# Optimization experiments

Hardware: AMD Instinct MI355X
Metric: run time of the kernel (lower is better)

Reference implementation:

```python
import jax, jax.numpy as jnp
import numpy as np

B, S, D, H = 2, 2048, 1024, 16
DK = D // H

def setup_inputs() -> dict:
    key = jax.random.key(0)
    ks = jax.random.split(key, 8)
    return {
        "query": jax.random.normal(ks[0], (B, S, D), dtype=jnp.float32),
        "key": jax.random.normal(ks[1], (B, S, D), dtype=jnp.float32),
        "value": jax.random.normal(ks[2], (B, S, D), dtype=jnp.float32),
        "mask": jax.random.randint(ks[3], (B, S, S), 0, 2, dtype=jnp.int32),
        "w_q": jax.random.normal(ks[4], (D, D), dtype=jnp.float32) * (D ** -0.5),
        "w_k": jax.random.normal(ks[5], (D, D), dtype=jnp.float32) * (D ** -0.5),
        "w_v": jax.random.normal(ks[6], (D, D), dtype=jnp.float32) * (D ** -0.5),
        "w_o": jax.random.normal(ks[7], (D, D), dtype=jnp.float32) * (D ** -0.5),
    }

def reference(query, key, value, mask, w_q, w_k, w_v, w_o):
    b, s, d = query.shape
    # Linear projections (torch nn.Linear: x @ W.T); here w_* are [out, in]
    Q = jnp.einsum('bsd,ed->bse', query, w_q).reshape(b, s, H, DK).transpose(0, 2, 1, 3)
    K = jnp.einsum('bsd,ed->bse', key, w_k).reshape(b, s, H, DK).transpose(0, 2, 1, 3)
    V = jnp.einsum('bsd,ed->bse', value, w_v).reshape(b, s, H, DK).transpose(0, 2, 1, 3)
    scale = jnp.float32(DK ** 0.5)
    scores = jnp.einsum('bhqd,bhkd->bhqk', Q, K) / scale  # [B,H,S,S]
    scores = jnp.where(mask[:, None, :, :] == 0, jnp.float32(-1e9), scores)
    attn = jax.nn.softmax(scores, axis=-1)  # dropout p=0 -> identity
    out = jnp.einsum('bhqk,bhkd->bhqd', attn, V)  # [B,H,S,DK]
    out = out.transpose(0, 2, 1, 3).reshape(b, s, d)
    return jnp.einsum('bsd,ed->bse', out, w_o)
```

## Files before the change

### kernel.cpp

```cpp
#include <hip/hip_runtime.h>
#include <stdint.h>

#define B_ 2
#define S_ 2048
#define D_ 1024
#define H_ 16
#define DK_ 64

typedef __attribute__((ext_vector_type(8))) short short8;
typedef __attribute__((ext_vector_type(4))) float f32x4;

__device__ __forceinline__ short f2bf(float f) {
    uint32_t u = __float_as_uint(f);
    return (short)((u + 0x7FFFu + ((u >> 16) & 1u)) >> 16);
}

__device__ __forceinline__ float fexp2(float x) {
    float r;
    asm("v_exp_f32 %0, %1" : "=v"(r) : "v"(x));
    return r;
}

__device__ __forceinline__ uint32_t cvt_pk_bf16(float lo, float hi) {
    uint32_t r;
    asm("v_cvt_pk_bf16_f32 %0, %1, %2" : "=v"(r) : "v"(lo), "v"(hi));
    return r;
}

#define GLOAD16(gptr, lptr)                                                      \
    __builtin_amdgcn_global_load_lds(                                            \
        (const __attribute__((address_space(1))) void*)(gptr),                   \
        (__attribute__((address_space(3))) void*)(lptr), 16, 0, 0)

__global__ __launch_bounds__(256) void cast_qkv(const float* __restrict__ a,
                                                const float* __restrict__ b,
                                                const float* __restrict__ c,
                                                short* __restrict__ oa,
                                                short* __restrict__ ob,
                                                short* __restrict__ oc) {
    int bid = blockIdx.x;
    int sel = bid >> 11;
    int i = (bid & 2047) * 256 + threadIdx.x;
    const float* in = (sel == 0) ? a : (sel == 1) ? b : c;
    short* out = (sel == 0) ? oa : (sel == 1) ? ob : oc;
    const float4* p = ((const float4*)in) + (size_t)i * 2;
    float4 x = p[0], y = p[1];
    short8 o;
    o[0] = f2bf(x.x); o[1] = f2bf(x.y); o[2] = f2bf(x.z); o[3] = f2bf(x.w);
    o[4] = f2bf(y.x); o[5] = f2bf(y.y); o[6] = f2bf(y.z); o[7] = f2bf(y.w);
    *(((short8*)out) + i) = o;
}

__global__ __launch_bounds__(256) void cast_w4(const float* __restrict__ a,
                                               const float* __restrict__ b,
                                               const float* __restrict__ c,
                                               const float* __restrict__ d,
                                               short* __restrict__ oa,
                                               short* __restrict__ ob,
                                               short* __restrict__ oc,
                                               short* __restrict__ od) {
    int bid = blockIdx.x;
    int sel = bid >> 9;
    int i = (bid & 511) * 256 + threadIdx.x;
    const float* in = (sel == 0) ? a : (sel == 1) ? b : (sel == 2) ? c : d;
    short* out = (sel == 0) ? oa : (sel == 1) ? ob : (sel == 2) ? oc : od;
    const float4* p = ((const float4*)in) + (size_t)i * 2;
    float4 x = p[0], y = p[1];
    short8 o;
    o[0] = f2bf(x.x); o[1] = f2bf(x.y); o[2] = f2bf(x.z); o[3] = f2bf(x.w);
    o[4] = f2bf(y.x); o[5] = f2bf(y.y); o[6] = f2bf(y.z); o[7] = f2bf(y.w);
    *(((short8*)out) + i) = o;
}

__global__ __launch_bounds__(256) void pack_mask(const int* __restrict__ mask,
                                                 uint32_t* __restrict__ packed,
                                                 float* __restrict__ lut) {
    if (blockIdx.x == 0 && threadIdx.x < 64) {
        int e = threadIdx.x >> 2, r = threadIdx.x & 3;
        lut[threadIdx.x] = __int_as_float(((e >> r) & 1) ? 0x7F800000u : 0xFF800000u);
    }
    size_t t = (size_t)blockIdx.x * 256 + threadIdx.x;
    int4 m = ((const int4*)mask)[t];
    uint32_t nib = (m.x != 0 ? 1u : 0u) | (m.y != 0 ? 2u : 0u) |
                   (m.z != 0 ? 4u : 0u) | (m.w != 0 ? 8u : 0u);
    int lane = threadIdx.x & 63;
    uint32_t v = nib << ((lane & 7) * 4);
    v |= __shfl_xor(v, 1);
    v |= __shfl_xor(v, 2);
    v |= __shfl_xor(v, 4);
    if ((lane & 7) == 0) packed[t >> 3] = v;
}

#define GEMM_BODY(A, W, C, F32OUT, Mv, Nv, Kv)                                              \
    __shared__ short As[128 * 32];                                                          \
    __shared__ short Bs[128 * 32];                                                          \
    const int tid = threadIdx.x;                                                            \
    const int lane = tid & 63;                                                              \
    const int w = tid >> 6;                                                                 \
    const int wm = w >> 1, wn = w & 1;                                                      \
    const int l_ = blockIdx.x + (blockIdx.y << 3);                                          \
    const int xcd_ = l_ & 7, ii_ = l_ >> 3;                                                 \
    const int mBase = ((xcd_ << 2) + (ii_ >> 3)) * 128;                                     \
    const int nBase = (ii_ & 7) * 128;                                                      \
    f32x4 acc[4][4];                                                                        \
    _Pragma("unroll") for (int i = 0; i < 4; i++)                                           \
        _Pragma("unroll") for (int j = 0; j < 4; j++) acc[i][j] = (f32x4)0.f;               \
    const int srow = lane >> 2;                                                             \
    const int sslot = lane & 3;                                                             \
    for (int k0 = 0; k0 < Kv; k0 += 32) {                                                   \
        _Pragma("unroll") for (int i = 0; i < 2; ++i) {                                     \
            int seg = w * 2 + i;                                                            \
            int row = seg * 16 + srow;                                                      \
            const short* ga = A + (size_t)(mBase + row) * Kv + k0 + sslot * 8;              \
            GLOAD16(ga, (char*)As + seg * 1024);                                            \
            const short* gb = W + (size_t)(nBase + row) * Kv + k0 + sslot * 8;              \
            GLOAD16(gb, (char*)Bs + seg * 1024);                                            \
        }                                                                                   \
        asm volatile("s_waitcnt vmcnt(0)" ::: "memory");                                    \
        __syncthreads();                                                                    \
        short8 af[4], bfv[4];                                                               \
        _Pragma("unroll") for (int mi = 0; mi < 4; mi++)                                    \
            af[mi] = *(const short8*)&As[(wm * 64 + mi * 16 + (lane & 15)) * 32 + (lane >> 4) * 8]; \
        _Pragma("unroll") for (int ni = 0; ni < 4; ni++)                                    \
            bfv[ni] = *(const short8*)&Bs[(wn * 64 + ni * 16 + (lane & 15)) * 32 + (lane >> 4) * 8]; \
        _Pragma("unroll") for (int mi = 0; mi < 4; mi++)                                    \
            _Pragma("unroll") for (int ni = 0; ni < 4; ni++)                                \
                acc[mi][ni] = __builtin_amdgcn_mfma_f32_16x16x32_bf16(af[mi], bfv[ni], acc[mi][ni], 0, 0, 0); \
        __syncthreads();                                                                    \
    }                                                                                       \
    _Pragma("unroll") for (int mi = 0; mi < 4; mi++)                                        \
        _Pragma("unroll") for (int ni = 0; ni < 4; ni++)                                    \
            _Pragma("unroll") for (int r = 0; r < 4; r++) {                                 \
                int row = mBase + wm * 64 + mi * 16 + (lane >> 4) * 4 + r;                  \
                int col = nBase + wn * 64 + ni * 16 + (lane & 15);                          \
                float v = acc[mi][ni][r];                                                   \
                if (F32OUT) ((float*)C)[(size_t)row * Nv + col] = v;                        \
                else        ((short*)C)[(size_t)row * Nv + col] = f2bf(v);                  \
            }

__global__ __launch_bounds__(256) void gemm3_nt(const short* __restrict__ A0, const short* __restrict__ W0, short* __restrict__ C0,
                                                const short* __restrict__ A1, const short* __restrict__ W1, short* __restrict__ C1,
                                                const short* __restrict__ A2, const short* __restrict__ W2, short* __restrict__ C2) {
    const int z = blockIdx.z;
    const short* A = (z == 0) ? A0 : (z == 1) ? A1 : A2;
    const short* W = (z == 0) ? W0 : (z == 1) ? W1 : W2;
    short* C = (z == 0) ? C0 : (z == 1) ? C1 : C2;
    GEMM_BODY(A, W, C, 0, (B_ * S_), D_, D_)
}

__global__ __launch_bounds__(256) void gemm_out(const short* __restrict__ A,
                                                const short* __restrict__ W,
                                                float* __restrict__ C) {
    GEMM_BODY(A, W, C, 1, (B_ * S_), D_, D_)
}

__global__ __launch_bounds__(256) void transpose_v(const short* __restrict__ Vp,
                                                   short* __restrict__ Vt) {
    __shared__ short t[64 * 72];
    int bid = blockIdx.x;
    int bh = bid >> 5;
    int st = bid & 31;
    int b = bh >> 4, h = bh & 15;
    int sBase = st * 64;
    int tid = threadIdx.x;
#pragma unroll
    for (int i = 0; i < 2; i++) {
        int ci = i * 256 + tid;
        int sr = ci >> 3, sl = ci & 7;
        short8 v = *(const short8*)&Vp[(size_t)(b * S_ + sBase + sr) * D_ + h * 64 + sl * 8];
#pragma unroll
        for (int j = 0; j < 8; j++) t[(sl * 8 + j) * 72 + sr] = v[j];
    }
    __syncthreads();
#pragma unroll
    for (int i = 0; i < 2; i++) {
        int ci = i * 256 + tid;
        int dk = ci >> 3, sl = ci & 7;
        short8 o = *(const short8*)&t[dk * 72 + sl * 8];
        *(short8*)&Vt[(size_t)((b * H_ + h) * 64 + dk) * S_ + sBase + sl * 8] = o;
    }
}

__global__ __launch_bounds__(256) void attn_kernel(const short* __restrict__ Qp,
                                                   const short* __restrict__ Kp,
                                                   const short* __restrict__ Vt,
                                                   const uint32_t* __restrict__ mp,
                                                   const float* __restrict__ lutg,
                                                   short* __restrict__ Op) {
    __shared__ short Ks[2][64 * 64];
    __shared__ short Vs[2][64 * 64];
    const int l_ = blockIdx.x + (blockIdx.y << 5);
    const int bh = ((l_ & 7) << 2) + (l_ >> 8);
    const int qt = (l_ >> 3) & 31;
    const int b = bh >> 4, h = bh & 15;
    const int qBase = qt * 64;
    const int tid = threadIdx.x, lane = tid & 63, w = tid >> 6;
    const int lg = lane >> 4;
    const int li = lane & 15;
    const float c1 = 0.18033688011112042f;

    const int q = qBase + w * 16 + li;

    short8 qf[2];
#pragma unroll
    for (int ks = 0; ks < 2; ks++)
        qf[ks] = *(const short8*)&Qp[(size_t)(b * S_ + q) * D_ + h * 64 + lg * 8 + ks * 32];

    const int r0 = tid >> 3, sl = tid & 7;
    const int gs = sl ^ (r0 & 7);
    const short* kg0 = Kp + ((size_t)(b * S_) + r0) * D_ + h * 64 + gs * 8;
    const short* kg1 = kg0 + (size_t)32 * D_;
    const short* vg0 = Vt + ((size_t)bh * 64 + r0) * S_ + gs * 8;
    const short* vg1 = vg0 + (size_t)32 * S_;
    const uint32_t* mrow = mp + ((size_t)(b * S_) + q) * 64;
    char* ldsK = (char*)&Ks[0][0];
    char* ldsV = (char*)&Vs[0][0];
    const int woff = w * 1024;

    GLOAD16(kg0, ldsK + woff);
    GLOAD16(kg1, ldsK + 4096 + woff);
    GLOAD16(vg0, ldsV + woff);
    GLOAD16(vg1, ldsV + 4096 + woff);
    uint2 mw = *(const uint2*)mrow;
    asm volatile("s_waitcnt vmcnt(0)" ::: "memory");
    __syncthreads();

    float m_r = -1e30f, l_r = 0.f;
    f32x4 acc[4];
#pragma unroll
    for (int g = 0; g < 4; g++) acc[g] = (f32x4)0.f;

    int cur = 0;

    for (int kt = 0; kt < S_ / 64; ++kt) {
        f32x4 msk[4];
#pragma unroll
        for (int nt = 0; nt < 4; nt++) {
            uint32_t wd = (nt < 2) ? mw.x : mw.y;
            uint32_t nib = (wd >> (((nt & 1) << 4) + (lg << 2))) & 0xFu;
            msk[nt] = *(const f32x4*)&lutg[nib * 4];
        }

        uint2 mwn;
        if (kt < S_ / 64 - 1) {
            const size_t ko = (size_t)((kt + 1) * 64) * D_;
            const int vo = (kt + 1) * 64;
            const int boff = (cur ^ 1) * 8192 + woff;
            GLOAD16(kg0 + ko, ldsK + boff);
            GLOAD16(kg1 + ko, ldsK + boff + 4096);
            GLOAD16(vg0 + vo, ldsV + boff);
            GLOAD16(vg1 + vo, ldsV + boff + 4096);
            mwn = *(const uint2*)&mrow[(kt + 1) * 2];
        }

        f32x4 sc[4];
        __builtin_amdgcn_s_setprio(1);
#pragma unroll
        for (int nt = 0; nt < 4; nt++) {
            f32x4 c = (f32x4)0.f;
#pragma unroll
            for (int ks = 0; ks < 2; ks++) {
                short8 kf = *(const short8*)&Ks[cur][(nt * 16 + li) * 64 + (((lg + ks * 4) ^ (li & 7)) << 3)];
                c = __builtin_amdgcn_mfma_f32_16x16x32_bf16(kf, qf[ks], c, 0, 0, 0);
            }
            sc[nt] = c;
        }
        __builtin_amdgcn_s_setprio(0);

        float tm = fmaxf(fmaxf(fmaxf(sc[0][0], sc[0][1]), fmaxf(sc[0][2], sc[0][3])),
                         fmaxf(fmaxf(sc[1][0], sc[1][1]), fmaxf(sc[1][2], sc[1][3])));
        tm = fmaxf(tm, fmaxf(fmaxf(fmaxf(sc[2][0], sc[2][1]), fmaxf(sc[2][2], sc[2][3])),
                             fmaxf(fmaxf(sc[3][0], sc[3][1]), fmaxf(sc[3][2], sc[3][3]))));
        tm = fmaxf(tm, __shfl_xor(tm, 16));
        tm = fmaxf(tm, __shfl_xor(tm, 32));

        if (__any((tm - m_r) * c1 > 10.0f)) {
            float mn = fmaxf(m_r, tm);
            float alpha = fexp2((m_r - mn) * c1);
            m_r = mn;
            l_r *= alpha;
#pragma unroll
            for (int g = 0; g < 4; g++) acc[g] *= alpha;
        }
        float mc = m_r * c1;

        uint32_t u[4][2];
        float ls = 0.f;
#pragma unroll
        for (int nt = 0; nt < 4; nt++) {
            float e0 = fexp2(fminf(__builtin_fmaf(sc[nt][0], c1, -mc), msk[nt][0]));
            float e1 = fexp2(fminf(__builtin_fmaf(sc[nt][1], c1, -mc), msk[nt][1]));
            float e2 = fexp2(fminf(__builtin_fmaf(sc[nt][2], c1, -mc), msk[nt][2]));
            float e3 = fexp2(fminf(__builtin_fmaf(sc[nt][3], c1, -mc), msk[nt][3]));
            ls += (e0 + e1) + (e2 + e3);
            u[nt][0] = cvt_pk_bf16(e0, e1);
            u[nt][1] = cvt_pk_bf16(e2, e3);
        }
        ls += __shfl_xor(ls, 16);
        ls += __shfl_xor(ls, 32);
        l_r += ls;

        __builtin_amdgcn_s_setprio(1);
#pragma unroll
        for (int ks = 0; ks < 2; ks++) {
            const uint32_t s00 = u[2 * ks][0], s01 = u[2 * ks][1];
            const uint32_t s10 = u[2 * ks + 1][0], s11 = u[2 * ks + 1][1];
            uint32_t e0 = (lg & 1) ? s00 : s10;
            uint32_t e1 = (lg & 1) ? s01 : s11;
            uint32_t x0 = (uint32_t)__shfl_xor((int)e0, 16);
            uint32_t x1 = (uint32_t)__shfl_xor((int)e1, 16);
            union { uint32_t w4[4]; short8 s8; } pu;
            pu.w4[0] = (lg & 1) ? x0 : s00;
            pu.w4[1] = (lg & 1) ? x1 : s01;
            pu.w4[2] = (lg & 1) ? s10 : x0;
            pu.w4[3] = (lg & 1) ? s11 : x1;
            const int f = ks * 4 + ((lg & 1) << 1) + (lg >> 1);
#pragma unroll
            for (int g = 0; g < 4; g++) {
                short8 vf = *(const short8*)&Vs[cur][(g * 16 + li) * 64 + ((f ^ (li & 7)) << 3)];
                acc[g] = __builtin_amdgcn_mfma_f32_16x16x32_bf16(vf, pu.s8, acc[g], 0, 0, 0);
            }
        }
        __builtin_amdgcn_s_setprio(0);

        asm volatile("s_waitcnt vmcnt(0)" ::: "memory");
        __syncthreads();
        cur ^= 1;
        if (kt < S_ / 64 - 1) mw = mwn;
    }

    float inv = 1.f / l_r;
    short* orow = &Op[(size_t)(b * S_ + q) * D_ + h * 64];
#pragma unroll
    for (int g = 0; g < 4; g++) {
        uint2 o;
        o.x = cvt_pk_bf16(acc[g][0] * inv, acc[g][1] * inv);
        o.y = cvt_pk_bf16(acc[g][2] * inv, acc[g][3] * inv);
        *(uint2*)&orow[g * 16 + lg * 4] = o;
    }
}

extern "C" void kernel_launch(void* const* d_in, const int* in_sizes, int n_in,
                              void* d_out, int out_size, void* d_ws, size_t ws_size,
                              hipStream_t stream) {
    const float* q  = (const float*)d_in[0];
    const float* k  = (const float*)d_in[1];
    const float* v  = (const float*)d_in[2];
    const int*   mk = (const int*)d_in[3];
    const float* wq = (const float*)d_in[4];
    const float* wk = (const float*)d_in[5];
    const float* wv = (const float*)d_in[6];
    const float* wo = (const float*)d_in[7];

    const size_t SZ = (size_t)B_ * S_ * D_;
    const size_t DD = (size_t)D_ * D_;
    const size_t NEED = (6 * SZ + 4 * DD) * 2 + (size_t)B_ * S_ * 64 * 4 + 256;
    if (ws_size < NEED) return;

    short* ws  = (short*)d_ws;
    short* qb  = ws;
    short* kb  = qb + SZ;
    short* vb  = kb + SZ;
    short* wqb = vb + SZ;
    short* wkb = wqb + DD;
    short* wvb = wkb + DD;
    short* wob = wvb + DD;
    short* Qp  = wob + DD;
    short* Kp  = Qp + SZ;
    short* Vp  = Kp + SZ;
    uint32_t* mp = (uint32_t*)(Vp + SZ);
    float* lutg = (float*)(mp + (size_t)B_ * S_ * 64);
    short* Vtr = qb;
    short* Opx = kb;

    dim3 blk(256);
    cast_qkv<<<dim3(3 * 2048), blk, 0, stream>>>(q, k, v, qb, kb, vb);
    cast_w4<<<dim3(4 * 512), blk, 0, stream>>>(wq, wk, wv, wo, wqb, wkb, wvb, wob);
    pack_mask<<<dim3((unsigned)((size_t)B_ * S_ * S_ / 4 / 256)), blk, 0, stream>>>(mk, mp, lutg);

    gemm3_nt<<<dim3(D_ / 128, B_ * S_ / 128, 3), blk, 0, stream>>>(
        qb, wqb, Qp, kb, wkb, Kp, vb, wvb, Vp);

    transpose_v<<<dim3(B_ * H_ * (S_ / 64)), blk, 0, stream>>>(Vp, Vtr);

    attn_kernel<<<dim3(32, 32), blk, 0, stream>>>(Qp, Kp, Vtr, mp, lutg, Opx);

    gemm_out<<<dim3(D_ / 128, B_ * S_ / 128), blk, 0, stream>>>(Opx, wob, (float*)d_out);
}
```

Measured before the change: 171.7 us.

## Fuse prep kernels, widen attention K/V tile to 128, fold mask into MFMA accumulator

Merges the three cast and mask-packing kernels into one prep launch, cutting launch overhead. The attention loop now processes 128 keys per iteration: two 64-row K/V sub-tiles per stage, double-buffered. The mask is applied as an additive bias (0 or -8e9) used as the MFMA initial accumulator, which removes the per-element fminf. This doubles LDS use per block and raises register pressure, which may reduce occupancy. Fully masked rows may also behave slightly differently from the -1e9 reference semantics.

Result: no change. 169.0 us (-1.5%).

```diff
diff --git a/kernel.cpp b/kernel.cpp
--- a/kernel.cpp
+++ b/kernel.cpp
@@ -32,63 +32,60 @@
         (const __attribute__((address_space(1))) void*)(gptr),                   \
         (__attribute__((address_space(3))) void*)(lptr), 16, 0, 0)
 
-__global__ __launch_bounds__(256) void cast_qkv(const float* __restrict__ a,
-                                                const float* __restrict__ b,
-                                                const float* __restrict__ c,
-                                                short* __restrict__ oa,
-                                                short* __restrict__ ob,
-                                                short* __restrict__ oc) {
+__global__ __launch_bounds__(256) void prep(const float* __restrict__ q,
+                                            const float* __restrict__ k,
+                                            const float* __restrict__ v,
+                                            const float* __restrict__ wq,
+                                            const float* __restrict__ wk,
+                                            const float* __restrict__ wv,
+                                            const float* __restrict__ wo,
+                                            const int* __restrict__ mask,
+                                            short* __restrict__ qb, short* __restrict__ kb,
+                                            short* __restrict__ vb,
+                                            short* __restrict__ wqb, short* __restrict__ wkb,
+                                            short* __restrict__ wvb, short* __restrict__ wob,
+                                            uint32_t* __restrict__ packed,
+                                            float* __restrict__ lut) {
     int bid = blockIdx.x;
-    int sel = bid >> 11;
-    int i = (bid & 2047) * 256 + threadIdx.x;
-    const float* in = (sel == 0) ? a : (sel == 1) ? b : c;
-    short* out = (sel == 0) ? oa : (sel == 1) ? ob : oc;
-    const float4* p = ((const float4*)in) + (size_t)i * 2;
-    float4 x = p[0], y = p[1];
-    short8 o;
-    o[0] = f2bf(x.x); o[1] = f2bf(x.y); o[2] = f2bf(x.z); o[3] = f2bf(x.w);
-    o[4] = f2bf(y.x); o[5] = f2bf(y.y); o[6] = f2bf(y.z); o[7] = f2bf(y.w);
-    *(((short8*)out) + i) = o;
-}
-
-__global__ __launch_bounds__(256) void cast_w4(const float* __restrict__ a,
-                                               const float* __restrict__ b,
-                                               const float* __restrict__ c,
-                                               const float* __restrict__ d,
-                                               short* __restrict__ oa,
-                                               short* __restrict__ ob,
-                                               short* __restrict__ oc,
-                                               short* __restrict__ od) {
-    int bid = blockIdx.x;
-    int sel = bid >> 9;
-    int i = (bid & 511) * 256 + threadIdx.x;
-    const float* in = (sel == 0) ? a : (sel == 1) ? b : (sel == 2) ? c : d;
-    short* out = (sel == 0) ? oa : (sel == 1) ? ob : (sel == 2) ? oc : od;
-    const float4* p = ((const float4*)in) + (size_t)i * 2;
-    float4 x = p[0], y = p[1];
-    short8 o;
-    o[0] = f2bf(x.x); o[1] = f2bf(x.y); o[2] = f2bf(x.z); o[3] = f2bf(x.w);
-    o[4] = f2bf(y.x); o[5] = f2bf(y.y); o[6] = f2bf(y.z); o[7] = f2bf(y.w);
-    *(((short8*)out) + i) = o;
-}
-
-__global__ __launch_bounds__(256) void pack_mask(const int* __restrict__ mask,
-                                                 uint32_t* __restrict__ packed,
-                                                 float* __restrict__ lut) {
-    if (blockIdx.x == 0 && threadIdx.x < 64) {
-        int e = threadIdx.x >> 2, r = threadIdx.x & 3;
-        lut[threadIdx.x] = __int_as_float(((e >> r) & 1) ? 0x7F800000u : 0xFF800000u);
-    }
-    size_t t = (size_t)blockIdx.x * 256 + threadIdx.x;
-    int4 m = ((const int4*)mask)[t];
-    uint32_t nib = (m.x != 0 ? 1u : 0u) | (m.y != 0 ? 2u : 0u) |
-                   (m.z != 0 ? 4u : 0u) | (m.w != 0 ? 8u : 0u);
-    int lane = threadIdx.x & 63;
-    uint32_t v = nib << ((lane & 7) * 4);
-    v |= __shfl_xor(v, 1);
-    v |= __shfl_xor(v, 2);
-    v |= __shfl_xor(v, 4);
-    if ((lane & 7) == 0) packed[t >> 3] = v;
+    int tid = threadIdx.x;
+    if (bid < 8192) {
+        const float* in;
+        short* out;
+        int i;
+        if (bid < 6144) {
+            int sel = bid >> 11;
+            i = (bid & 2047) * 256 + tid;
+            in = (sel == 0) ? q : (sel == 1) ? k : v;
+            out = (sel == 0) ? qb : (sel == 1) ? kb : vb;
+        } else {
+            int idx = bid - 6144;
+            int sel = idx >> 9;
+            i = (idx & 511) * 256 + tid;
+            in = (sel == 0) ? wq : (sel == 1) ? wk : (sel == 2) ? wv : wo;
+            out = (sel == 0) ? wqb : (sel == 1) ? wkb : (sel == 2) ? wvb : wob;
+            if (idx == 0 && tid < 64) {
+                int e = tid >> 2, r = tid & 3;
+                lut[tid] = ((e >> r) & 1) ? 0.0f : -8.0e9f;
+            }
+        }
+        const float4* p = ((const float4*)in) + (size_t)i * 2;
+        float4 x = p[0], y = p[1];
+        short8 o;
+        o[0] = f2bf(x.x); o[1] = f2bf(x.y); o[2] = f2bf(x.z); o[3] = f2bf(x.w);
+        o[4] = f2bf(y.x); o[5] = f2bf(y.y); o[6] = f2bf(y.z); o[7] = f2bf(y.w);
+        *(((short8*)out) + i) = o;
+    } else {
+        size_t t = (size_t)(bid - 8192) * 256 + tid;
+        int4 m = ((const int4*)mask)[t];
+        uint32_t nib = (m.x != 0 ? 1u : 0u) | (m.y != 0 ? 2u : 0u) |
+                       (m.z != 0 ? 4u : 0u) | (m.w != 0 ? 8u : 0u);
+        int lane = tid & 63;
+        uint32_t vv = nib << ((lane & 7) * 4);
+        vv |= __shfl_xor(vv, 1);
+        vv |= __shfl_xor(vv, 2);
+        vv |= __shfl_xor(vv, 4);
+        if ((lane & 7) == 0) packed[t >> 3] = vv;
+    }
 }
 
 #define GEMM_BODY(A, W, C, F32OUT, Mv, Nv, Kv)                                              \
@@ -187,8 +184,8 @@
                                                    const uint32_t* __restrict__ mp,
                                                    const float* __restrict__ lutg,
                                                    short* __restrict__ Op) {
-    __shared__ short Ks[2][64 * 64];
-    __shared__ short Vs[2][64 * 64];
+    __shared__ short Ks[2][2][64 * 64];
+    __shared__ short Vs[2][2][64 * 64];
     const int l_ = blockIdx.x + (blockIdx.y << 5);
     const int bh = ((l_ & 7) << 2) + (l_ >> 8);
     const int qt = (l_ >> 3) & 31;
@@ -208,20 +205,21 @@
 
     const int r0 = tid >> 3, sl = tid & 7;
     const int gs = sl ^ (r0 & 7);
-    const short* kg0 = Kp + ((size_t)(b * S_) + r0) * D_ + h * 64 + gs * 8;
-    const short* kg1 = kg0 + (size_t)32 * D_;
-    const short* vg0 = Vt + ((size_t)bh * 64 + r0) * S_ + gs * 8;
-    const short* vg1 = vg0 + (size_t)32 * S_;
+    const short* kgb = Kp + ((size_t)(b * S_) + r0) * D_ + h * 64 + gs * 8;
+    const short* vgb = Vt + ((size_t)bh * 64 + r0) * S_ + gs * 8;
     const uint32_t* mrow = mp + ((size_t)(b * S_) + q) * 64;
-    char* ldsK = (char*)&Ks[0][0];
-    char* ldsV = (char*)&Vs[0][0];
+    char* ldsK = (char*)&Ks[0][0][0];
+    char* ldsV = (char*)&Vs[0][0][0];
     const int woff = w * 1024;
 
-    GLOAD16(kg0, ldsK + woff);
-    GLOAD16(kg1, ldsK + 4096 + woff);
-    GLOAD16(vg0, ldsV + woff);
-    GLOAD16(vg1, ldsV + 4096 + woff);
-    uint2 mw = *(const uint2*)mrow;
+#pragma unroll
+    for (int st = 0; st < 2; st++) {
+        GLOAD16(kgb + (size_t)(st * 64) * D_, ldsK + st * 8192 + woff);
+        GLOAD16(kgb + (size_t)(st * 64 + 32) * D_, ldsK + st * 8192 + 4096 + woff);
+        GLOAD16(vgb + st * 64, ldsV + st * 8192 + woff);
+        GLOAD16(vgb + st * 64 + (size_t)32 * S_, ldsV + st * 8192 + 4096 + woff);
+    }
+    uint4 mw4 = *(const uint4*)mrow;
     asm volatile("s_waitcnt vmcnt(0)" ::: "memory");
     __syncthreads();
 
@@ -232,45 +230,56 @@
 
     int cur = 0;
 
-    for (int kt = 0; kt < S_ / 64; ++kt) {
-        f32x4 msk[4];
-#pragma unroll
-        for (int nt = 0; nt < 4; nt++) {
-            uint32_t wd = (nt < 2) ? mw.x : mw.y;
+    for (int kt = 0; kt < S_ / 128; ++kt) {
+        uint32_t mwarr[4] = {mw4.x, mw4.y, mw4.z, mw4.w};
+        f32x4 msk[8];
+#pragma unroll
+        for (int nt = 0; nt < 8; nt++) {
+            uint32_t wd = mwarr[nt >> 1];
             uint32_t nib = (wd >> (((nt & 1) << 4) + (lg << 2))) & 0xFu;
             msk[nt] = *(const f32x4*)&lutg[nib * 4];
         }
 
-        uint2 mwn;
-        if (kt < S_ / 64 - 1) {
-            const size_t ko = (size_t)((kt + 1) * 64) * D_;
-            const int vo = (kt + 1) * 64;
-            const int boff = (cur ^ 1) * 8192 + woff;
-            GLOAD16(kg0 + ko, ldsK + boff);
-            GLOAD16(kg1 + ko, ldsK + boff + 4096);
-            GLOAD16(vg0 + vo, ldsV + boff);
-            GLOAD16(vg1 + vo, ldsV + boff + 4096);
-            mwn = *(const uint2*)&mrow[(kt + 1) * 2];
-        }
-
-        f32x4 sc[4];
+        uint4 mwn;
+        if (kt < S_ / 128 - 1) {
+            const int boff = (cur ^ 1) * 16384 + woff;
+#pragma unroll
+            for (int st = 0; st < 2; st++) {
+                const size_t kr = (size_t)((kt + 1) * 128 + st * 64);
+                GLOAD16(kgb + kr * D_, ldsK + boff + st * 8192);
+                GLOAD16(kgb + (kr + 32) * D_, ldsK + boff + st * 8192 + 4096);
+                GLOAD16(vgb + kr, ldsV + boff + st * 8192);
+                GLOAD16(vgb + kr + (size_t)32 * S_, ldsV + boff + st * 8192 + 4096);
+            }
+            mwn = *(const uint4*)&mrow[(kt + 1) * 4];
+        }
+
+        f32x4 sc[8];
         __builtin_amdgcn_s_setprio(1);
 #pragma unroll
-        for (int nt = 0; nt < 4; nt++) {
-            f32x4 c = (f32x4)0.f;
-#pragma unroll
-            for (int ks = 0; ks < 2; ks++) {
-                short8 kf = *(const short8*)&Ks[cur][(nt * 16 + li) * 64 + (((lg + ks * 4) ^ (li & 7)) << 3)];
-                c = __builtin_amdgcn_mfma_f32_16x16x32_bf16(kf, qf[ks], c, 0, 0, 0);
-            }
-            sc[nt] = c;
-        }
+        for (int st = 0; st < 2; st++)
+#pragma unroll
+            for (int ntl = 0; ntl < 4; ntl++) {
+                f32x4 c = msk[st * 4 + ntl];
+#pragma unroll
+                for (int ks = 0; ks < 2; ks++) {
+                    short8 kf = *(const short8*)&Ks[cur][st][(ntl * 16 + li) * 64 + (((lg + ks * 4) ^ (li & 7)) << 3)];
+                    c = __builtin_amdgcn_mfma_f32_16x16x32_bf16(kf, qf[ks], c, 0, 0, 0);
+                }
+                sc[st * 4 + ntl] = c;
+            }
         __builtin_amdgcn_s_setprio(0);
 
-        float tm = fmaxf(fmaxf(fmaxf(sc[0][0], sc[0][1]), fmaxf(sc[0][2], sc[0][3])),
-                         fmaxf(fmaxf(sc[1][0], sc[1][1]), fmaxf(sc[1][2], sc[1][3])));
-        tm = fmaxf(tm, fmaxf(fmaxf(fmaxf(sc[2][0], sc[2][1]), fmaxf(sc[2][2], sc[2][3])),
-                             fmaxf(fmaxf(sc[3][0], sc[3][1]), fmaxf(sc[3][2], sc[3][3]))));
+        float t0 = fmaxf(fmaxf(sc[0][0], sc[0][1]), fmaxf(sc[0][2], sc[0][3]));
+        float t1 = fmaxf(fmaxf(sc[1][0], sc[1][1]), fmaxf(sc[1][2], sc[1][3]));
+        float t2 = fmaxf(fmaxf(sc[2][0], sc[2][1]), fmaxf(sc[2][2], sc[2][3]));
+        float t3 = fmaxf(fmaxf(sc[3][0], sc[3][1]), fmaxf(sc[3][2], sc[3][3]));
+        float t4 = fmaxf(fmaxf(sc[4][0], sc[4][1]), fmaxf(sc[4][2], sc[4][3]));
+        float t5 = fmaxf(fmaxf(sc[5][0], sc[5][1]), fmaxf(sc[5][2], sc[5][3]));
+        float t6 = fmaxf(fmaxf(sc[6][0], sc[6][1]), fmaxf(sc[6][2], sc[6][3]));
+        float t7 = fmaxf(fmaxf(sc[7][0], sc[7][1]), fmaxf(sc[7][2], sc[7][3]));
+        float tm = fmaxf(fmaxf(fmaxf(t0, t1), fmaxf(t2, t3)),
+                         fmaxf(fmaxf(t4, t5), fmaxf(t6, t7)));
         tm = fmaxf(tm, __shfl_xor(tm, 16));
         tm = fmaxf(tm, __shfl_xor(tm, 32));
 
@@ -284,14 +293,14 @@
         }
         float mc = m_r * c1;
 
-        uint32_t u[4][2];
+        uint32_t u[8][2];
         float ls = 0.f;
 #pragma unroll
-        for (int nt = 0; nt < 4; nt++) {
-            float e0 = fexp2(fminf(__builtin_fmaf(sc[nt][0], c1, -mc), msk[nt][0]));
-            float e1 = fexp2(fminf(__builtin_fmaf(sc[nt][1], c1, -mc), msk[nt][1]));
-            float e2 = fexp2(fminf(__builtin_fmaf(sc[nt][2], c1, -mc), msk[nt][2]));
-            float e3 = fexp2(fminf(__builtin_fmaf(sc[nt][3], c1, -mc), msk[nt][3]));
+        for (int nt = 0; nt < 8; nt++) {
+            float e0 = fexp2(__builtin_fmaf(sc[nt][0], c1, -mc));
+            float e1 = fexp2(__builtin_fmaf(sc[nt][1], c1, -mc));
+            float e2 = fexp2(__builtin_fmaf(sc[nt][2], c1, -mc));
+            float e3 = fexp2(__builtin_fmaf(sc[nt][3], c1, -mc));
             ls += (e0 + e1) + (e2 + e3);
             u[nt][0] = cvt_pk_bf16(e0, e1);
             u[nt][1] = cvt_pk_bf16(e2, e3);
@@ -302,7 +311,7 @@
 
         __builtin_amdgcn_s_setprio(1);
 #pragma unroll
-        for (int ks = 0; ks < 2; ks++) {
+        for (int ks = 0; ks < 4; ks++) {
             const uint32_t s00 = u[2 * ks][0], s01 = u[2 * ks][1];
             const uint32_t s10 = u[2 * ks + 1][0], s11 = u[2 * ks + 1][1];
             uint32_t e0 = (lg & 1) ? s00 : s10;
@@ -315,9 +324,10 @@
             pu.w4[2] = (lg & 1) ? s10 : x0;
             pu.w4[3] = (lg & 1) ? s11 : x1;
             const int f = ks * 4 + ((lg & 1) << 1) + (lg >> 1);
+            const int stv = f >> 3, fl = f & 7;
 #pragma unroll
             for (int g = 0; g < 4; g++) {
-                short8 vf = *(const short8*)&Vs[cur][(g * 16 + li) * 64 + ((f ^ (li & 7)) << 3)];
+                short8 vf = *(const short8*)&Vs[cur][stv][(g * 16 + li) * 64 + ((fl ^ (li & 7)) << 3)];
                 acc[g] = __builtin_amdgcn_mfma_f32_16x16x32_bf16(vf, pu.s8, acc[g], 0, 0, 0);
             }
         }
@@ -326,7 +336,7 @@
         asm volatile("s_waitcnt vmcnt(0)" ::: "memory");
         __syncthreads();
         cur ^= 1;
-        if (kt < S_ / 64 - 1) mw = mwn;
+        if (kt < S_ / 128 - 1) mw4 = mwn;
     }
 
     float inv = 1.f / l_r;
@@ -374,16 +384,14 @@
     short* Opx = kb;
 
     dim3 blk(256);
-    cast_qkv<<<dim3(3 * 2048), blk, 0, stream>>>(q, k, v, qb, kb, vb);
-    cast_w4<<<dim3(4 * 512), blk, 0, stream>>>(wq, wk, wv, wo, wqb, wkb, wvb, wob);
-    pack_mask<<<dim3((unsigned)((size_t)B_ * S_ * S_ / 4 / 256)), blk, 0, stream>>>(mk, mp, lutg);
-
-    gemm3_nt<<<dim3(D_ / 128, B_ * S_ / 128, 3), blk, 0, stream>>>(
-        qb, wqb, Qp, kb, wkb, Kp, vb, wvb, Vp);
+    prep<<<dim3(16384), blk, 0, stream>>>(q, k, v, wq, wk, wv, wo, mk,
+                                          qb, kb, vb, wqb, wkb, wvb, wob, mp, lutg);
+
+    gemm3_nt<<<dim3(8, 32, 3), blk, 0, stream>>>(qb, wqb, Qp, kb, wkb, Kp, vb, wvb, Vp);
 
     transpose_v<<<dim3(B_ * H_ * (S_ / 64)), blk, 0, stream>>>(Vp, Vtr);
 
     attn_kernel<<<dim3(32, 32), blk, 0, stream>>>(Qp, Kp, Vtr, mp, lutg, Opx);
 
-    gemm_out<<<dim3(D_ / 128, B_ * S_ / 128), blk, 0, stream>>>(Opx, wob, (float*)d_out);
-}
+    gemm_out<<<dim3(8, 32), blk, 0, stream>>>(Opx, wob, (float*)d_out);
+}
```
